# Optimization experiments

Hardware: AMD Instinct MI355X
Metric: run time of the kernel (lower is better)

The kernel has to match this reference:

```python
import jax, jax.numpy as jnp
import numpy as np

B, S, D, L, H = 4, 2048, 1024, 2, 8  # batch, seq, d_model, hierarchy levels, heads
DH = D // H


def _ln(x, g, b, eps=1e-5):
    mu = jnp.mean(x, axis=-1, keepdims=True)
    xc = x - mu
    var = jnp.mean(xc * xc, axis=-1, keepdims=True)
    return xc * jax.lax.rsqrt(var + eps) * g + b


def setup_inputs() -> dict:
    key = jax.random.key(0)
    ks = jax.random.split(key, 16)
    s = 0.02
    f32 = jnp.float32
    return {
        "x": jax.random.normal(ks[0], (B, S, D), f32),
        "hierarchy_levels": jax.random.randint(ks[1], (B, S), 0, 3),
        # per-level processor MLPs (stacked over level axis)
        "p1_w": jax.random.normal(ks[2], (L, D, D), f32) * s,
        "p1_b": jnp.zeros((L, D), f32),
        "p2_w": jax.random.normal(ks[3], (L, D, D), f32) * s,
        "p2_b": jnp.zeros((L, D), f32),
        "ln_g": jnp.ones((L, D), f32),
        "ln_b": jnp.zeros((L, D), f32),
        # multihead attention projections
        "wq": jax.random.normal(ks[4], (D, D), f32) * s,
        "bq": jnp.zeros((D,), f32),
        "wk": jax.random.normal(ks[5], (D, D), f32) * s,
        "bk": jnp.zeros((D,), f32),
        "wv": jax.random.normal(ks[6], (D, D), f32) * s,
        "bv": jnp.zeros((D,), f32),
        "wo": jax.random.normal(ks[7], (D, D), f32) * s,
        "bo": jnp.zeros((D,), f32),
        # integration MLP: Linear(L*D -> D), SiLU, Linear(D -> D), LayerNorm
        "i1_w": jax.random.normal(ks[8], (L * D, D), f32) * s,
        "i1_b": jnp.zeros((D,), f32),
        "i2_w": jax.random.normal(ks[9], (D, D), f32) * s,
        "i2_b": jnp.zeros((D,), f32),
        "iln_g": jnp.ones((D,), f32),
        "iln_b": jnp.zeros((D,), f32),
    }


def reference(x, hierarchy_levels, p1_w, p1_b, p2_w, p2_b, ln_g, ln_b,
              wq, bq, wk, bk, wv, bv, wo, bo,
              i1_w, i1_b, i2_w, i2_b, iln_g, iln_b):
    # --- per-token expert routing: compute all L processors, select by level ---
    t = jax.nn.silu(jnp.einsum('bsd,lde->lbse', x, p1_w) + p1_b[:, None, None, :])
    h = jnp.einsum('lbse,led->lbsd', t, p2_w) + p2_b[:, None, None, :]
    h = _ln(h, ln_g[:, None, None, :], ln_b[:, None, None, :])  # [L,B,S,D]
    oh = jax.nn.one_hot(hierarchy_levels, L, dtype=x.dtype)      # [B,S,L]; level>=L -> all-zero row
    hsel = jnp.einsum('lbsd,bsl->bsd', h, oh)                    # [B,S,D]
    # --- self-attention over routed outputs ---
    q = (hsel @ wq + bq).reshape(B, S, H, DH)
    k = (hsel @ wk + bk).reshape(B, S, H, DH)
    v = (hsel @ wv + bv).reshape(B, S, H, DH)
    scores = jnp.einsum('bqhd,bkhd->bhqk', q, k) / np.sqrt(DH).astype(x.dtype)
    a = jax.nn.softmax(scores, axis=-1)                          # [B,H,S,S]
    ctx = jnp.einsum('bhqk,bkhd->bqhd', a, v).reshape(B, S, D)
    attended = ctx @ wo + bo
    attn_weights = jnp.mean(a, axis=1)                           # torch avg over heads: [B,S,S]
    # --- integration MLP ---
    z = jnp.concatenate([hsel, attended], axis=-1)               # [B,S,2D]
    z = jax.nn.silu(z @ i1_w + i1_b) @ i2_w + i2_b
    out = _ln(z, iln_g, iln_b)
    return out, attn_weights
```

## Files before the change

kernel.cpp:

```cpp
#include <hip/hip_runtime.h>
#include <cstdint>
#include <cstddef>

#define B_ 4
#define S_ 2048
#define D_ 1024
#define H_ 8
#define DH_ 128
#define MTOT 8192
#define NT_ 32
#define SCALE2 (0.08838834764831845f * 1.4426950408889634f)

typedef __attribute__((ext_vector_type(8))) short s16x8;
typedef __attribute__((ext_vector_type(4))) float f32x4;
typedef __attribute__((ext_vector_type(8))) __bf16 bf16x8;

static __device__ __forceinline__ f32x4 mfma16(s16x8 a, s16x8 b, f32x4 c) {
  return __builtin_amdgcn_mfma_f32_16x16x32_bf16(
      __builtin_bit_cast(bf16x8, a), __builtin_bit_cast(bf16x8, b), c, 0, 0, 0);
}
static __device__ __forceinline__ unsigned short f2bf(float f) {
  unsigned u = __builtin_bit_cast(unsigned, f);
  u += 0x7fffu + ((u >> 16) & 1u);
  return (unsigned short)(u >> 16);
}
static __device__ __forceinline__ float bf2f(unsigned short u) {
  return __builtin_bit_cast(float, (unsigned)u << 16);
}
static __device__ __forceinline__ unsigned cvtpk2(float a, float b) {
  unsigned r;
  asm("v_cvt_pk_bf16_f32 %0, %1, %2" : "=v"(r) : "v"(a), "v"(b));
  return r;
}
static __device__ __forceinline__ void gload_lds16(const void* g, void* l) {
  __builtin_amdgcn_global_load_lds(
      (__attribute__((address_space(1))) void*)(void*)(g),
      (__attribute__((address_space(3))) void*)(l), 16, 0, 0);
}

__global__ __launch_bounds__(256) void xconv_kernel(const float* __restrict__ x,
                                                    unsigned short* __restrict__ xb) {
  long i = ((long)blockIdx.x * 256 + threadIdx.x) * 4;
  float4 v = *(const float4*)(x + i);
  ushort4 o;
  o.x = f2bf(v.x); o.y = f2bf(v.y); o.z = f2bf(v.z); o.w = f2bf(v.w);
  *(ushort4*)(xb + i) = o;
}

__global__ __launch_bounds__(256) void route_kernel(const int* __restrict__ levels,
                                                    int* __restrict__ cnt,
                                                    int* __restrict__ ridx,
                                                    int* __restrict__ act,
                                                    int* __restrict__ act2) {
  const int row = blockIdx.x * 256 + threadIdx.x;
  const int lane = threadIdx.x & 63;
  const int lvl = levels[row];
  const unsigned long long lmlt = (lane == 63) ? ~0ULL >> 1 : (1ULL << lane) - 1;

#pragma unroll
  for (int c = 0; c < 2; c++) {
    bool pred = (lvl == c);
    unsigned long long mask = __ballot(pred);
    int total = __popcll(mask);
    if (total) {
      int leader = __ffsll((long long)mask) - 1;
      int base = 0;
      if (lane == leader) base = atomicAdd(&cnt[c], total);
      base = __shfl(base, leader);
      if (pred) ridx[c * MTOT + base + __popcll(mask & lmlt)] = row;
    }
  }
  {
    bool pred = (lvl < 2);
    unsigned long long mask = __ballot(pred);
    int total = __popcll(mask);
    if (total) {
      int leader = __ffsll((long long)mask) - 1;
      int base = 0;
      if (lane == leader) base = atomicAdd(&cnt[2], total);
      base = __shfl(base, leader);
      if (pred) act[base + __popcll(mask & lmlt)] = row;
    }
    unsigned long long mask2 = ~mask;
    int total2 = 64 - total;
    if (total2) {
      int leader2 = __ffsll((long long)mask2) - 1;
      int base2 = 0;
      if (lane == leader2) base2 = atomicAdd(&cnt[3], total2);
      base2 = __shfl(base2, leader2);
      if (!pred) act2[base2 + __popcll(mask2 & lmlt)] = row;
    }
  }
}

__global__ __launch_bounds__(256) void lvl2fill_kernel(
    const int* __restrict__ act2, const int* __restrict__ cntp,
    const float* __restrict__ bq, const float* __restrict__ bk,
    const float* __restrict__ bv,
    unsigned short* __restrict__ qb, unsigned short* __restrict__ kb,
    unsigned short* __restrict__ vb, unsigned short* __restrict__ z) {
  const int idx = blockIdx.x;
  if (idx >= *cntp) return;
  const long row = act2[idx];
  const int t = threadIdx.x;
  const float4 q4 = *(const float4*)(bq + t * 4);
  const float4 k4 = *(const float4*)(bk + t * 4);
  const float4 v4 = *(const float4*)(bv + t * 4);
  ushort4 qo, ko, vo;
  qo.x = f2bf(q4.x * SCALE2); qo.y = f2bf(q4.y * SCALE2);
  qo.z = f2bf(q4.z * SCALE2); qo.w = f2bf(q4.w * SCALE2);
  ko.x = f2bf(k4.x); ko.y = f2bf(k4.y); ko.z = f2bf(k4.z); ko.w = f2bf(k4.w);
  vo.x = f2bf(v4.x); vo.y = f2bf(v4.y); vo.z = f2bf(v4.z); vo.w = f2bf(v4.w);
  *(ushort4*)(qb + row * 1024 + t * 4) = qo;
  *(ushort4*)(kb + row * 1024 + t * 4) = ko;
  *(ushort4*)(vb + row * 1024 + t * 4) = vo;
  *(ushort4*)(z + row * 2048 + t * 4) = (ushort4){0, 0, 0, 0};
}

struct WtDesc { const float* src; unsigned short* dst; long dst_ld; long dst_off; };
struct WtArgs { WtDesc d[10]; };
__global__ __launch_bounds__(256) void wtrans_all_kernel(WtArgs a) {
  __shared__ unsigned short tile[32][33];
  const int wi = blockIdx.y >> 5;
  const WtDesc de = a.d[wi];
  int r0 = (blockIdx.y & 31) * 32, c0 = blockIdx.x * 32;
  int tr = threadIdx.x >> 5, tc = threadIdx.x & 31;
#pragma unroll
  for (int i = 0; i < 4; i++)
    tile[tr + i * 8][tc] = f2bf(de.src[(long)(r0 + tr + i * 8) * 1024 + c0 + tc]);
  __syncthreads();
#pragma unroll
  for (int i = 0; i < 4; i++)
    de.dst[(long)(c0 + tr + i * 8) * de.dst_ld + de.dst_off + r0 + tc] = tile[tc][tr + i * 8];
}

__global__ __launch_bounds__(256) void vtrans_kernel(const unsigned short* __restrict__ V,
                                                     unsigned short* __restrict__ Vt) {
  __shared__ unsigned short tile[32][33];
  int b = blockIdx.z;
  int h = blockIdx.y >> 2, d0 = (blockIdx.y & 3) * 32;
  int s0 = blockIdx.x * 32;
  int tr = threadIdx.x >> 5, tc = threadIdx.x & 31;
#pragma unroll
  for (int i = 0; i < 4; i++)
    tile[tr + i * 8][tc] = V[((long)(b * S_) + s0 + tr + i * 8) * D_ + h * DH_ + d0 + tc];
  __syncthreads();
  const int sk = s0 + tc;
  const int k6 = sk & 63;
  const int slot = ((k6 >> 5) << 5) | (((k6 >> 2) & 3) << 3) | (((k6 >> 4) & 1) << 2) | (k6 & 3);
  const int ss = (sk & ~63) | slot;
#pragma unroll
  for (int i = 0; i < 4; i++)
    Vt[((long)(b * H_ + h) * DH_ + d0 + tr + i * 8) * S_ + ss] = tile[tc][tr + i * 8];
}

template <int TAG>
__global__ __launch_bounds__(256) void gemm_kernel(
    const unsigned short* __restrict__ A, int lda,
    const unsigned short* __restrict__ Wt, int ldw,
    const float* __restrict__ bias, float oscale,
    unsigned short* __restrict__ Cb, float* __restrict__ Cf, int ldc,
    int K, int do_silu) {
  __shared__ unsigned short lA[128 * 64];
  __shared__ unsigned short lB[128 * 64];
  const int t = threadIdx.x;
  const int wid = t >> 6, lane = t & 63;
  const int g = lane >> 4, lc = lane & 15;
  const int wr = wid >> 1, wc = wid & 1;
  const int nwg = gridDim.x * gridDim.y;
  int flat = blockIdx.x + gridDim.x * blockIdx.y;
  flat = (flat & 7) * (nwg >> 3) + (flat >> 3);
  const int m0 = (flat / gridDim.x) * 128;
  const int n0 = (flat % gridDim.x) * 128;
  const int srow = lane >> 3, scol = lane & 7;
  const int sxor = (scol ^ srow) << 4;

  f32x4 acc[4][4];
#pragma unroll
  for (int i = 0; i < 4; i++)
#pragma unroll
    for (int j = 0; j < 4; j++) acc[i][j] = (f32x4){0.f, 0.f, 0.f, 0.f};

  const int nk = K >> 6;
  for (int kt = 0; kt < nk; ++kt) {
    const int k0 = kt << 6;
#pragma unroll
    for (int i = 0; i < 4; i++) {
      const int r0 = wid * 32 + i * 8;
      gload_lds16((const char*)(A + (m0 + r0 + srow) * (long)lda + k0) + sxor,
                  (char*)lA + r0 * 128);
      gload_lds16((const char*)(Wt + (n0 + r0 + srow) * (long)ldw + k0) + sxor,
                  (char*)lB + r0 * 128);
    }
    __syncthreads();
#pragma unroll
    for (int kk = 0; kk < 2; kk++) {
      s16x8 af[4], bfr[4];
#pragma unroll
      for (int i = 0; i < 4; i++) {
        int row = wr * 64 + i * 16 + lc;
        af[i] = *(const s16x8*)((const char*)lA + row * 128 +
                                ((kk * 64 + g * 16) ^ ((row & 7) << 4)));
      }
#pragma unroll
      for (int j = 0; j < 4; j++) {
        int row = wc * 64 + j * 16 + lc;
        bfr[j] = *(const s16x8*)((const char*)lB + row * 128 +
                                 ((kk * 64 + g * 16) ^ ((row & 7) << 4)));
      }
#pragma unroll
      for (int i = 0; i < 4; i++)
#pragma unroll
        for (int j = 0; j < 4; j++) acc[i][j] = mfma16(af[i], bfr[j], acc[i][j]);
    }
    __syncthreads();
  }
#pragma unroll
  for (int i = 0; i < 4; i++) {
    const long rbase = m0 + wr * 64 + i * 16 + g * 4;
#pragma unroll
    for (int j = 0; j < 4; j++) {
      const int col = n0 + wc * 64 + j * 16 + lc;
      const float bv = bias[col];
#pragma unroll
      for (int r = 0; r < 4; r++) {
        float v = (acc[i][j][r] + bv) * oscale;
        if (do_silu) v = v / (1.f + __expf(-v));
        if (Cb) Cb[(rbase + r) * (long)ldc + col] = f2bf(v);
        else Cf[(rbase + r) * (long)ldc + col] = v;
      }
    }
  }
}

template <int TAG>
__global__ __launch_bounds__(512) void gemm8_kernel(
    const unsigned short* __restrict__ A, int lda,
    const unsigned short* __restrict__ Wt, int ldw,
    const float* __restrict__ bias, float oscale,
    unsigned short* __restrict__ Cb, int ldc,
    int K, int do_silu) {
  __shared__ unsigned short lA[128 * 64];
  __shared__ unsigned short lB[128 * 64];
  const int t = threadIdx.x;
  const int wid = t >> 6, lane = t & 63;
  const int g = lane >> 4, lc = lane & 15;
  const int wr = wid >> 1, wc = wid & 1;
  const int nwg = gridDim.x * gridDim.y;
  int flat = blockIdx.x + gridDim.x * blockIdx.y;
  flat = (flat & 7) * (nwg >> 3) + (flat >> 3);
  const int m0 = (flat / gridDim.x) * 128;
  const int n0 = (flat % gridDim.x) * 128;
  const int srow = lane >> 3, scol = lane & 7;
  const int sxor = (scol ^ srow) << 4;

  f32x4 acc[2][4];
#pragma unroll
  for (int i = 0; i < 2; i++)
#pragma unroll
    for (int j = 0; j < 4; j++) acc[i][j] = (f32x4){0.f, 0.f, 0.f, 0.f};

  const int nk = K >> 6;
  for (int kt = 0; kt < nk; ++kt) {
    const int k0 = kt << 6;
#pragma unroll
    for (int i = 0; i < 2; i++) {
      const int r0 = wid * 16 + i * 8;
      gload_lds16((const char*)(A + (m0 + r0 + srow) * (long)lda + k0) + sxor,
                  (char*)lA + r0 * 128);
      gload_lds16((const char*)(Wt + (n0 + r0 + srow) * (long)ldw + k0) + sxor,
                  (char*)lB + r0 * 128);
    }
    __syncthreads();
#pragma unroll
    for (int kk = 0; kk < 2; kk++) {
      s16x8 af[2], bfr[4];
#pragma unroll
      for (int i = 0; i < 2; i++) {
        int row = wr * 32 + i * 16 + lc;
        af[i] = *(const s16x8*)((const char*)lA + row * 128 +
                                ((kk * 64 + g * 16) ^ ((row & 7) << 4)));
      }
#pragma unroll
      for (int j = 0; j < 4; j++) {
        int row = wc * 64 + j * 16 + lc;
        bfr[j] = *(const s16x8*)((const char*)lB + row * 128 +
                                 ((kk * 64 + g * 16) ^ ((row & 7) << 4)));
      }
#pragma unroll
      for (int i = 0; i < 2; i++)
#pragma unroll
        for (int j = 0; j < 4; j++) acc[i][j] = mfma16(af[i], bfr[j], acc[i][j]);
    }
    __syncthreads();
  }
#pragma unroll
  for (int i = 0; i < 2; i++) {
    const long rbase = m0 + wr * 32 + i * 16 + g * 4;
#pragma unroll
    for (int j = 0; j < 4; j++) {
      const int col = n0 + wc * 64 + j * 16 + lc;
      const float bv = bias[col];
#pragma unroll
      for (int r = 0; r < 4; r++) {
        float v = (acc[i][j][r] + bv) * oscale;
        if (do_silu) v = v / (1.f + __expf(-v));
        Cb[(rbase + r) * (long)ldc + col] = f2bf(v);
      }
    }
  }
}

template <int RMAP>
__global__ __launch_bounds__(512) void gemm8_moe_kernel(
    const unsigned short* __restrict__ A, int lda,
    const unsigned short* __restrict__ Wt0, int ldw,
    const float* __restrict__ bias0,
    unsigned short* __restrict__ Cb, int ldc,
    int K, int do_silu, const int* __restrict__ ridx, const int* __restrict__ cnt2) {
  __shared__ unsigned short lA[128 * 64];
  __shared__ unsigned short lB[128 * 64];
  const int t = threadIdx.x;
  const int wid = t >> 6, lane = t & 63;
  const int g = lane >> 4, lc = lane & 15;
  const int wr = wid >> 1, wc = wid & 1;
  const int nwg = gridDim.x * gridDim.y;
  int flat = blockIdx.x + gridDim.x * blockIdx.y;
  flat = (flat & 7) * (nwg >> 3) + (flat >> 3);
  const int m0 = (flat / gridDim.x) * 128;
  const int n0 = (flat % gridDim.x) * 128;
  const int lvl = m0 >> 12;
  const int lm0 = m0 & 4095;
  if (lm0 >= cnt2[lvl]) return;
  const unsigned short* Wt = Wt0 + (long)lvl * 1048576;
  const float* bias = bias0 + lvl * 1024;
  const int srow = lane >> 3, scol = lane & 7;
  const int sxor = (scol ^ srow) << 4;

  const unsigned short* abase[2];
#pragma unroll
  for (int i = 0; i < 2; i++) {
    int ar;
    if (RMAP) ar = ridx[lvl * MTOT + lm0 + wid * 16 + i * 8 + srow];
    else ar = m0 + wid * 16 + i * 8 + srow;
    abase[i] = A + (long)ar * lda;
  }

  f32x4 acc[2][4];
#pragma unroll
  for (int i = 0; i < 2; i++)
#pragma unroll
    for (int j = 0; j < 4; j++) acc[i][j] = (f32x4){0.f, 0.f, 0.f, 0.f};

  const int nk = K >> 6;
  for (int kt = 0; kt < nk; ++kt) {
    const int k0 = kt << 6;
#pragma unroll
    for (int i = 0; i < 2; i++) {
      const int r0 = wid * 16 + i * 8;
      gload_lds16((const char*)(abase[i] + k0) + sxor, (char*)lA + r0 * 128);
      gload_lds16((const char*)(Wt + (n0 + r0 + srow) * (long)ldw + k0) + sxor,
                  (char*)lB + r0 * 128);
    }
    __syncthreads();
#pragma unroll
    for (int kk = 0; kk < 2; kk++) {
      s16x8 af[2], bfr[4];
#pragma unroll
      for (int i = 0; i < 2; i++) {
        int row = wr * 32 + i * 16 + lc;
        af[i] = *(const s16x8*)((const char*)lA + row * 128 +
                                ((kk * 64 + g * 16) ^ ((row & 7) << 4)));
      }
#pragma unroll
      for (int j = 0; j < 4; j++) {
        int row = wc * 64 + j * 16 + lc;
        bfr[j] = *(const s16x8*)((const char*)lB + row * 128 +
                                 ((kk * 64 + g * 16) ^ ((row & 7) << 4)));
      }
#pragma unroll
      for (int i = 0; i < 2; i++)
#pragma unroll
        for (int j = 0; j < 4; j++) acc[i][j] = mfma16(af[i], bfr[j], acc[i][j]);
    }
    __syncthreads();
  }
#pragma unroll
  for (int i = 0; i < 2; i++) {
    const long rbase = m0 + wr * 32 + i * 16 + g * 4;
#pragma unroll
    for (int j = 0; j < 4; j++) {
      const int col = n0 + wc * 64 + j * 16 + lc;
      const float bv = bias[col];
#pragma unroll
      for (int r = 0; r < 4; r++) {
        float v = acc[i][j][r] + bv;
        if (do_silu) v = v / (1.f + __expf(-v));
        Cb[(rbase + r) * (long)ldc + col] = f2bf(v);
      }
    }
  }
}

__global__ __launch_bounds__(256) void wct_gemm_kernel(
    const unsigned short* __restrict__ A,
    const unsigned short* __restrict__ Wb,
    float* __restrict__ Cf) {
  __shared__ unsigned short lA[128 * 64];
  __shared__ unsigned short lB[128 * 64];
  const int t = threadIdx.x;
  const int wid = t >> 6, lane = t & 63;
  const int g = lane >> 4, lc = lane & 15;
  const int wr = wid >> 1, wc = wid & 1;
  const int chunk = blockIdx.y >> 3;
  const int m0 = (blockIdx.y & 7) * 128;
  const int n0 = blockIdx.x * 128;
  const unsigned short* A0 = A + chunk * 256;
  const unsigned short* W0 = Wb + chunk * 256;
  float* C0 = Cf + (long)chunk * 1048576;
  const int srow = lane >> 3, scol = lane & 7;
  const int sxor = (scol ^ srow) << 4;

  f32x4 acc[4][4];
#pragma unroll
  for (int i = 0; i < 4; i++)
#pragma unroll
    for (int j = 0; j < 4; j++) acc[i][j] = (f32x4){0.f, 0.f, 0.f, 0.f};

  for (int kt = 0; kt < 4; ++kt) {
    const int k0 = kt << 6;
#pragma unroll
    for (int i = 0; i < 4; i++) {
      const int r0 = wid * 32 + i * 8;
      gload_lds16((const char*)(A0 + (m0 + r0 + srow) * 2048L + k0) + sxor,
                  (char*)lA + r0 * 128);
      gload_lds16((const char*)(W0 + (n0 + r0 + srow) * 1024L + k0) + sxor,
                  (char*)lB + r0 * 128);
    }
    __syncthreads();
#pragma unroll
    for (int kk = 0; kk < 2; kk++) {
      s16x8 af[4], bfr[4];
#pragma unroll
      for (int i = 0; i < 4; i++) {
        int row = wr * 64 + i * 16 + lc;
        af[i] = *(const s16x8*)((const char*)lA + row * 128 +
                                ((kk * 64 + g * 16) ^ ((row & 7) << 4)));
      }
#pragma unroll
      for (int j = 0; j < 4; j++) {
        int row = wc * 64 + j * 16 + lc;
        bfr[j] = *(const s16x8*)((const char*)lB + row * 128 +
                                 ((kk * 64 + g * 16) ^ ((row & 7) << 4)));
      }
#pragma unroll
      for (int i = 0; i < 4; i++)
#pragma unroll
        for (int j = 0; j < 4; j++) acc[i][j] = mfma16(af[i], bfr[j], acc[i][j]);
    }
    __syncthreads();
  }
#pragma unroll
  for (int i = 0; i < 4; i++) {
    const long rbase = m0 + wr * 64 + i * 16 + g * 4;
#pragma unroll
    for (int j = 0; j < 4; j++) {
      const int col = n0 + wc * 64 + j * 16 + lc;
#pragma unroll
      for (int r = 0; r < 4; r++) C0[(rbase + r) * 1024L + col] = acc[i][j][r];
    }
  }
}

__global__ __launch_bounds__(256) void wct_reduce_kernel(
    const float* __restrict__ hraw, unsigned short* __restrict__ i1t) {
  long e = ((long)blockIdx.x * 256 + threadIdx.x) * 2;
  float a0 = hraw[e] + hraw[e + 1048576] + hraw[e + 2097152] + hraw[e + 3145728];
  float a1 = hraw[e + 1] + hraw[e + 1 + 1048576] + hraw[e + 1 + 2097152] +
             hraw[e + 1 + 3145728];
  unsigned pk = cvtpk2(a0, a1);
  long n = e >> 10, c = e & 1023;
  *(unsigned*)(i1t + n * 2048 + 1024 + c) = pk;
}

__global__ __launch_bounds__(256) void biascomb_kernel(
    const unsigned short* __restrict__ i1t, const float* __restrict__ bo,
    const float* __restrict__ i1b, float* __restrict__ bias_c) {
  const int n = blockIdx.x, t = threadIdx.x;
  ushort4 w = *(const ushort4*)(i1t + (long)n * 2048 + 1024 + t * 4);
  float4 b = *(const float4*)(bo + t * 4);
  float s = bf2f(w.x) * b.x + bf2f(w.y) * b.y + bf2f(w.z) * b.z + bf2f(w.w) * b.w;
#pragma unroll
  for (int m = 32; m; m >>= 1) s += __shfl_xor(s, m);
  __shared__ float ws_[4];
  if ((t & 63) == 0) ws_[t >> 6] = s;
  __syncthreads();
  if (t == 0) bias_c[n] = i1b[n] + ws_[0] + ws_[1] + ws_[2] + ws_[3];
}

__global__ __launch_bounds__(256) void ln_moe_kernel(
    const unsigned short* __restrict__ in, const int* __restrict__ ridx,
    const int* __restrict__ cnt2,
    const float* __restrict__ gg0, const float* __restrict__ bb0,
    unsigned short* __restrict__ outb, long ldo) {
  const int row = blockIdx.x;
  const int lvl = row >> 12;
  const int lrow = row & 4095;
  if (lrow >= cnt2[lvl]) return;
  const int orow = ridx[lvl * MTOT + lrow];
  const float* gg = gg0 + lvl * 1024;
  const float* bb = bb0 + lvl * 1024;
  const int t = threadIdx.x;
  const ushort4 u = *(const ushort4*)(in + (long)row * D_ + t * 4);
  float v0 = bf2f(u.x), v1 = bf2f(u.y), v2 = bf2f(u.z), v3 = bf2f(u.w);
  float s1 = v0 + v1 + v2 + v3;
  float s2 = v0 * v0 + v1 * v1 + v2 * v2 + v3 * v3;
#pragma unroll
  for (int m = 32; m; m >>= 1) {
    s1 += __shfl_xor(s1, m);
    s2 += __shfl_xor(s2, m);
  }
  __shared__ float w1[4], w2[4];
  if ((t & 63) == 0) { w1[t >> 6] = s1; w2[t >> 6] = s2; }
  __syncthreads();
  s1 = w1[0] + w1[1] + w1[2] + w1[3];
  s2 = w2[0] + w2[1] + w2[2] + w2[3];
  const float mu = s1 * (1.f / D_);
  const float var = s2 * (1.f / D_) - mu * mu;
  const float rs = rsqrtf(var + 1e-5f);
  float vv[4] = {v0, v1, v2, v3};
#pragma unroll
  for (int jj = 0; jj < 4; jj++) {
    int col = t * 4 + jj;
    float y = (vv[jj] - mu) * rs * gg[col] + bb[col];
    outb[(long)orow * ldo + col] = f2bf(y);
  }
}

__global__ __launch_bounds__(256) void ln_kernel(
    const unsigned short* __restrict__ in,
    const float* __restrict__ gg, const float* __restrict__ bb,
    float* __restrict__ outf) {
  const int row = blockIdx.x;
  const int t = threadIdx.x;
  const ushort4 u = *(const ushort4*)(in + (long)row * D_ + t * 4);
  float v0 = bf2f(u.x), v1 = bf2f(u.y), v2 = bf2f(u.z), v3 = bf2f(u.w);
  float s1 = v0 + v1 + v2 + v3;
  float s2 = v0 * v0 + v1 * v1 + v2 * v2 + v3 * v3;
#pragma unroll
  for (int m = 32; m; m >>= 1) {
    s1 += __shfl_xor(s1, m);
    s2 += __shfl_xor(s2, m);
  }
  __shared__ float w1[4], w2[4];
  if ((t & 63) == 0) { w1[t >> 6] = s1; w2[t >> 6] = s2; }
  __syncthreads();
  s1 = w1[0] + w1[1] + w1[2] + w1[3];
  s2 = w2[0] + w2[1] + w2[2] + w2[3];
  const float mu = s1 * (1.f / D_);
  const float var = s2 * (1.f / D_) - mu * mu;
  const float rs = rsqrtf(var + 1e-5f);
  float vv[4] = {v0, v1, v2, v3};
#pragma unroll
  for (int jj = 0; jj < 4; jj++) {
    int col = t * 4 + jj;
    outf[(long)row * D_ + col] = (vv[jj] - mu) * rs * gg[col] + bb[col];
  }
}

__global__ __launch_bounds__(256) void gemm_qkv_kernel(
    const unsigned short* __restrict__ A, int lda,
    const unsigned short* __restrict__ Wt,
    const float* __restrict__ bq, const float* __restrict__ bk,
    const float* __restrict__ bv,
    unsigned short* __restrict__ qb, unsigned short* __restrict__ kb,
    unsigned short* __restrict__ vb,
    const int* __restrict__ act, const int* __restrict__ cntp) {
  __shared__ unsigned short lA[128 * 64];
  __shared__ unsigned short lB[128 * 64];
  const int t = threadIdx.x;
  const int wid = t >> 6, lane = t & 63;
  const int g = lane >> 4, lc = lane & 15;
  const int wr = wid >> 1, wc = wid & 1;
  const int nwg = gridDim.x * gridDim.y;
  int flat = blockIdx.x + gridDim.x * blockIdx.y;
  flat = (flat & 7) * (nwg >> 3) + (flat >> 3);
  const int m0 = (flat / gridDim.x) * 128;
  const int n0 = (flat % gridDim.x) * 128;
  if (m0 >= *cntp) return;
  const int srow = lane >> 3, scol = lane & 7;
  const int sxor = (scol ^ srow) << 4;

  const unsigned short* abase[4];
#pragma unroll
  for (int i = 0; i < 4; i++)
    abase[i] = A + (long)act[m0 + wid * 32 + i * 8 + srow] * lda;

  f32x4 acc[4][4];
#pragma unroll
  for (int i = 0; i < 4; i++)
#pragma unroll
    for (int j = 0; j < 4; j++) acc[i][j] = (f32x4){0.f, 0.f, 0.f, 0.f};

  for (int kt = 0; kt < 16; ++kt) {
    const int k0 = kt << 6;
#pragma unroll
    for (int i = 0; i < 4; i++) {
      const int r0 = wid * 32 + i * 8;
      gload_lds16((const char*)(abase[i] + k0) + sxor, (char*)lA + r0 * 128);
      gload_lds16((const char*)(Wt + (n0 + r0 + srow) * 1024 + k0) + sxor,
                  (char*)lB + r0 * 128);
    }
    __syncthreads();
#pragma unroll
    for (int kk = 0; kk < 2; kk++) {
      s16x8 af[4], bfr[4];
#pragma unroll
      for (int i = 0; i < 4; i++) {
        int row = wr * 64 + i * 16 + lc;
        af[i] = *(const s16x8*)((const char*)lA + row * 128 +
                                ((kk * 64 + g * 16) ^ ((row & 7) << 4)));
      }
#pragma unroll
      for (int j = 0; j < 4; j++) {
        int row = wc * 64 + j * 16 + lc;
        bfr[j] = *(const s16x8*)((const char*)lB + row * 128 +
                                 ((kk * 64 + g * 16) ^ ((row & 7) << 4)));
      }
#pragma unroll
      for (int i = 0; i < 4; i++)
#pragma unroll
        for (int j = 0; j < 4; j++) acc[i][j] = mfma16(af[i], bfr[j], acc[i][j]);
    }
    __syncthreads();
  }
  const int whichB = n0 >> 10;
  const float* bias = whichB == 0 ? bq : whichB == 1 ? bk : bv;
  unsigned short* Cb = whichB == 0 ? qb : whichB == 1 ? kb : vb;
  const float oscale = whichB == 0 ? (float)SCALE2 : 1.0f;
  const int nb = n0 & 1023;
#pragma unroll
  for (int i = 0; i < 4; i++) {
    const int ribase = m0 + wr * 64 + i * 16 + g * 4;
#pragma unroll
    for (int j = 0; j < 4; j++) {
      const int col = nb + wc * 64 + j * 16 + lc;
      const float bvv = bias[col];
#pragma unroll
      for (int r = 0; r < 4; r++) {
        float v = (acc[i][j][r] + bvv) * oscale;
        Cb[(long)act[ribase + r] * 1024L + col] = f2bf(v);
      }
    }
  }
}

__global__ __launch_bounds__(256, 2) void flash_kernel(
    const unsigned short* __restrict__ Q, const unsigned short* __restrict__ Kb,
    const unsigned short* __restrict__ Vt,
    unsigned short* __restrict__ zatt, float* __restrict__ Mo, float* __restrict__ Lo) {
  __shared__ unsigned short lK[2][64 * 128];
  __shared__ unsigned short lV[2][128 * 64];
  const int t = threadIdx.x, wid = t >> 6, lane = t & 63;
  const int g = lane >> 4, lc = lane & 15;
  const int d = blockIdx.x + 16 * (blockIdx.y + 8 * blockIdx.z);
  const int qd = d >> 3, rd = d & 7;
  const int grp = rd + 8 * (qd >> 4);
  const int b = grp >> 3, h = grp & 7, q0 = (qd & 15) * 128;
  const int k_l4 = lane >> 4, k_c = lane & 15;
  const int v_l3 = lane >> 3, v_c = lane & 7;

  s16x8 qf[2][4];
#pragma unroll
  for (int qi = 0; qi < 2; qi++)
#pragma unroll
    for (int kk = 0; kk < 4; kk++)
      qf[qi][kk] = *(const s16x8*)(Q +
          ((long)(b * S_ + q0 + wid * 32 + qi * 16 + lc)) * D_ + h * DH_ + kk * 32 + g * 8);

  f32x4 acco[2][8];
#pragma unroll
  for (int qi = 0; qi < 2; qi++)
#pragma unroll
    for (int dn = 0; dn < 8; dn++) acco[qi][dn] = (f32x4){0.f, 0.f, 0.f, 0.f};
  float m_run[2] = {-1e30f, -1e30f}, l_run[2] = {0.f, 0.f};

  auto stageK = [&](int kt, int buf) {
#pragma unroll
    for (int i = 0; i < 4; i++) {
      const int r0 = wid * 16 + i * 4;
      const int row = r0 + k_l4;
      gload_lds16((const char*)(Kb + (b * S_ + kt * 64 + row) * D_ + h * DH_) +
                      ((k_c ^ (row & 7)) << 4),
                  (char*)&lK[buf][0] + r0 * 256);
    }
  };
  auto stageV = [&](int kt, int buf) {
#pragma unroll
    for (int i = 0; i < 4; i++) {
      const int r0 = wid * 32 + i * 8;
      const int row = r0 + v_l3;
      gload_lds16((const char*)(Vt + ((b * H_ + h) * DH_ + row) * S_ + kt * 64) +
                      ((v_c ^ (row & 7)) << 4),
                  (char*)&lV[buf][0] + r0 * 128);
    }
  };

  stageK(0, 0);
  stageV(0, 0);
  __syncthreads();

  for (int kt = 0; kt < NT_; ++kt) {
    const int cur = kt & 1;
    if (kt + 1 < NT_) { stageK(kt + 1, cur ^ 1); stageV(kt + 1, cur ^ 1); }

    f32x4 s[2][4];
#pragma unroll
    for (int qi = 0; qi < 2; qi++)
#pragma unroll
      for (int kn = 0; kn < 4; kn++) s[qi][kn] = (f32x4){0.f, 0.f, 0.f, 0.f};
    __builtin_amdgcn_s_setprio(1);
#pragma unroll
    for (int kk = 0; kk < 4; kk++) {
      s16x8 kf[4];
#pragma unroll
      for (int kn = 0; kn < 4; kn++) {
        int row = kn * 16 + lc;
        kf[kn] = *(const s16x8*)((const char*)&lK[cur][0] + row * 256 +
                                 ((kk * 64 + g * 16) ^ ((row & 7) << 4)));
      }
#pragma unroll
      for (int qi = 0; qi < 2; qi++)
#pragma unroll
        for (int kn = 0; kn < 4; kn++) s[qi][kn] = mfma16(kf[kn], qf[qi][kk], s[qi][kn]);
    }
    __builtin_amdgcn_s_setprio(0);

    float mx[2];
    int trig = 0;
#pragma unroll
    for (int qi = 0; qi < 2; qi++) {
      float m01 = fmaxf(fmaxf(s[qi][0][0], s[qi][0][1]), fmaxf(s[qi][0][2], s[qi][0][3]));
      float m1 = fmaxf(fmaxf(s[qi][1][0], s[qi][1][1]), fmaxf(s[qi][1][2], s[qi][1][3]));
      float m2 = fmaxf(fmaxf(s[qi][2][0], s[qi][2][1]), fmaxf(s[qi][2][2], s[qi][2][3]));
      float m3 = fmaxf(fmaxf(s[qi][3][0], s[qi][3][1]), fmaxf(s[qi][3][2], s[qi][3][3]));
      float m = fmaxf(fmaxf(m01, m1), fmaxf(m2, m3));
      m = fmaxf(m, __shfl_xor(m, 16));
      m = fmaxf(m, __shfl_xor(m, 32));
      mx[qi] = m;
      trig |= (m > m_run[qi] + 8.0f);
    }
    if (__any(trig)) {
#pragma unroll
      for (int qi = 0; qi < 2; qi++) {
        float mn = fmaxf(m_run[qi], mx[qi]);
        float fsc = exp2f(m_run[qi] - mn);
        m_run[qi] = mn;
        l_run[qi] *= fsc;
#pragma unroll
        for (int dn = 0; dn < 8; dn++)
#pragma unroll
          for (int r = 0; r < 4; r++) acco[qi][dn][r] *= fsc;
      }
    }

    unsigned w[2][4][2];
#pragma unroll
    for (int qi = 0; qi < 2; qi++) {
      float ls = 0.f;
#pragma unroll
      for (int kn = 0; kn < 4; kn++) {
        float p0 = exp2f(s[qi][kn][0] - m_run[qi]);
        float p1 = exp2f(s[qi][kn][1] - m_run[qi]);
        float p2 = exp2f(s[qi][kn][2] - m_run[qi]);
        float p3 = exp2f(s[qi][kn][3] - m_run[qi]);
        ls += (p0 + p1) + (p2 + p3);
        w[qi][kn][0] = cvtpk2(p0, p1);
        w[qi][kn][1] = cvtpk2(p2, p3);
      }
      ls += __shfl_xor(ls, 16);
      ls += __shfl_xor(ls, 32);
      l_run[qi] += ls;
    }

    __builtin_amdgcn_s_setprio(1);
#pragma unroll
    for (int kk = 0; kk < 2; kk++) {
      s16x8 pf[2];
#pragma unroll
      for (int qi = 0; qi < 2; qi++) {
        union { unsigned u[4]; s16x8 v; } pu;
        pu.u[0] = w[qi][2 * kk][0];
        pu.u[1] = w[qi][2 * kk][1];
        pu.u[2] = w[qi][2 * kk + 1][0];
        pu.u[3] = w[qi][2 * kk + 1][1];
        pf[qi] = pu.v;
      }
#pragma unroll
      for (int dn = 0; dn < 8; dn++) {
        int vrow = dn * 16 + lc;
        s16x8 vf = *(const s16x8*)((const char*)&lV[cur][0] + vrow * 128 +
                                   ((kk * 64 + g * 16) ^ ((vrow & 7) << 4)));
#pragma unroll
        for (int qi = 0; qi < 2; qi++) acco[qi][dn] = mfma16(vf, pf[qi], acco[qi][dn]);
      }
    }
    __builtin_amdgcn_s_setprio(0);
    __syncthreads();
  }

  char* tb = (char*)&lK[0][0] + wid * 8192;
#pragma unroll
  for (int qi = 0; qi < 2; qi++) {
    float inv = 1.f / l_run[qi];
    int row = qi * 16 + lc;
#pragma unroll
    for (int dn = 0; dn < 8; dn++) {
      unsigned lo = cvtpk2(acco[qi][dn][0] * inv, acco[qi][dn][1] * inv);
      unsigned hi = cvtpk2(acco[qi][dn][2] * inv, acco[qi][dn][3] * inv);
      unsigned long long pk = (unsigned long long)lo | ((unsigned long long)hi << 32);
      *(unsigned long long*)(tb + row * 256 + ((dn * 32 + g * 8) ^ ((row & 7) << 4))) = pk;
    }
  }
  __syncthreads();
#pragma unroll
  for (int i = 0; i < 8; i++) {
    const int row = i * 4 + (lane >> 4);
    const int chunk = lane & 15;
    s16x8 vv = *(const s16x8*)(tb + row * 256 + ((chunk * 16) ^ ((row & 7) << 4)));
    *(s16x8*)(zatt + ((long)(b * S_ + q0 + wid * 32 + row)) * 2048 + h * DH_ + chunk * 8) = vv;
  }
  if (g == 0) {
#pragma unroll
    for (int qi = 0; qi < 2; qi++) {
      int q = q0 + wid * 32 + qi * 16 + lc;
      Mo[(long)(b * H_ + h) * S_ + q] = m_run[qi];
      Lo[(long)(b * H_ + h) * S_ + q] = l_run[qi];
    }
  }
}

__global__ __launch_bounds__(256) void attw_kernel(
    const unsigned short* __restrict__ Q, const unsigned short* __restrict__ Kb,
    const float* __restrict__ Mo, const float* __restrict__ Lo,
    float* __restrict__ AW) {
  __shared__ unsigned short lK[2][128 * 128];
  __shared__ float lm[H_][128], winv[H_][128];
  const int t = threadIdx.x, wid = t >> 6, lane = t & 63;
  const int g = lane >> 4, lc = lane & 15;
  const int f = blockIdx.x + 16 * (blockIdx.y + 16 * blockIdx.z);
  const int xcd = f & 7, i_ = f >> 3;
  const int grp = (i_ >> 4) * 8 + xcd;
  const int b = grp >> 4, k0 = (grp & 15) * 128, q0 = (i_ & 15) * 128;
  const int k_l4 = lane >> 4, k_c = lane & 15;

  for (int i = t; i < H_ * 128; i += 256) {
    int h = i >> 7, qq = i & 127;
    lm[h][qq] = Mo[(long)(b * H_ + h) * S_ + q0 + qq];
    winv[h][qq] = 0.125f / Lo[(long)(b * H_ + h) * S_ + q0 + qq];
  }

  auto stageK = [&](int h, int buf) {
#pragma unroll
    for (int i = 0; i < 8; i++) {
      const int r0 = wid * 32 + i * 4;
      const int row = r0 + k_l4;
      gload_lds16((const char*)(Kb + ((long)(b * S_ + k0 + row)) * D_ + h * DH_) +
                      ((k_c ^ (row & 7)) << 4),
                  (char*)&lK[buf][0] + r0 * 256);
    }
  };

  f32x4 acc[2][8];
#pragma unroll
  for (int qi = 0; qi < 2; qi++)
#pragma unroll
    for (int kn = 0; kn < 8; kn++) acc[qi][kn] = (f32x4){0.f, 0.f, 0.f, 0.f};

  stageK(0, 0);
  __syncthreads();

  for (int h = 0; h < H_; ++h) {
    const int cur = h & 1;
    if (h + 1 < H_) stageK(h + 1, cur ^ 1);
    f32x4 s[2][8];
#pragma unroll
    for (int qi = 0; qi < 2; qi++)
#pragma unroll
      for (int kn = 0; kn < 8; kn++) s[qi][kn] = (f32x4){0.f, 0.f, 0.f, 0.f};
    __builtin_amdgcn_s_setprio(1);
#pragma unroll
    for (int kk = 0; kk < 4; kk++) {
      s16x8 qa[2];
#pragma unroll
      for (int qi = 0; qi < 2; qi++)
        qa[qi] = *(const s16x8*)(Q +
            ((long)(b * S_ + q0 + wid * 32 + qi * 16 + lc)) * D_ + h * DH_ + kk * 32 + g * 8);
#pragma unroll
      for (int kn = 0; kn < 8; kn++) {
        int row = kn * 16 + lc;
        s16x8 kf = *(const s16x8*)((const char*)&lK[cur][0] + row * 256 +
                                   ((kk * 64 + g * 16) ^ ((row & 7) << 4)));
#pragma unroll
        for (int qi = 0; qi < 2; qi++) s[qi][kn] = mfma16(qa[qi], kf, s[qi][kn]);
      }
    }
    __builtin_amdgcn_s_setprio(0);
#pragma unroll
    for (int qi = 0; qi < 2; qi++)
#pragma unroll
      for (int kn = 0; kn < 8; kn++)
#pragma unroll
        for (int r = 0; r < 4; r++) {
          int qq = wid * 32 + qi * 16 + g * 4 + r;
          acc[qi][kn][r] += exp2f(s[qi][kn][r] - lm[h][qq]) * winv[h][qq];
        }
    __syncthreads();
  }
#pragma unroll
  for (int qi = 0; qi < 2; qi++)
#pragma unroll
    for (int kn = 0; kn < 8; kn++)
#pragma unroll
      for (int r = 0; r < 4; r++) {
        long q = q0 + wid * 32 + qi * 16 + g * 4 + r;
        int k = k0 + kn * 16 + lc;
        AW[((long)b * S_ + q) * S_ + k] = acc[qi][kn][r];
      }
}

__global__ void signal_kernel(float* out, float v) { out[0] = v; }

extern "C" void kernel_launch(void* const* d_in, const int* in_sizes, int n_in,
                              void* d_out, int out_size, void* d_ws, size_t ws_size,
                              hipStream_t stream) {
  constexpr size_t OFF_XB = 0;
  constexpr size_t OFF_W = 16777216ULL;
  constexpr size_t OFF_T = 39845888ULL;
  constexpr size_t OFF_HR = 56623104ULL;
  constexpr size_t OFF_Z = 90177536ULL;
  constexpr size_t OFF_Q = 123731968ULL;
  constexpr size_t OFF_K = 140509184ULL;
  constexpr size_t OFF_V = 157286400ULL;
  constexpr size_t OFF_VT = 174063616ULL;
  constexpr size_t OFF_M = 190840832ULL;
  constexpr size_t OFF_L = 191102976ULL;
  constexpr size_t OFF_CNT = 191365120ULL;
  constexpr size_t OFF_RIDX = 191365184ULL;
  constexpr size_t OFF_BC = OFF_RIDX + 2ULL * MTOT * 4;
  constexpr size_t OFF_ACT = OFF_BC + 4096;
  constexpr size_t OFF_ACT2 = OFF_ACT + MTOT * 4;
  constexpr size_t WS_NEED = OFF_ACT2 + MTOT * 4;

  if (ws_size < WS_NEED) {
    signal_kernel<<<1, 1, 0, stream>>>((float*)d_out, (float)ws_size);
    return;
  }
  const float* x = (const float*)d_in[0];
  const int* levels = (const int*)d_in[1];
  const float* p1w = (const float*)d_in[2];
  const float* p1b = (const float*)d_in[3];
  const float* p2w = (const float*)d_in[4];
  const float* p2b = (const float*)d_in[5];
  const float* lng = (const float*)d_in[6];
  const float* lnb = (const float*)d_in[7];
  const float* wq = (const float*)d_in[8];
  const float* bq = (const float*)d_in[9];
  const float* wk = (const float*)d_in[10];
  const float* bk = (const float*)d_in[11];
  const float* wv = (const float*)d_in[12];
  const float* bv = (const float*)d_in[13];
  const float* wo = (const float*)d_in[14];
  const float* bo = (const float*)d_in[15];
  const float* i1w = (const float*)d_in[16];
  const float* i1b = (const float*)d_in[17];
  const float* i2w = (const float*)d_in[18];
  const float* i2b = (const float*)d_in[19];
  const float* ilng = (const float*)d_in[20];
  const float* ilnb = (const float*)d_in[21];

  char* ws = (char*)d_ws;
  unsigned short* xb = (unsigned short*)(ws + OFF_XB);
  unsigned short* p1t = (unsigned short*)(ws + OFF_W);
  unsigned short* p2t = p1t + 2 * 1048576;
  unsigned short* wqt = p2t + 2 * 1048576;
  unsigned short* wkt = wqt + 1048576;
  unsigned short* wvt = wkt + 1048576;
  unsigned short* wob = wvt + 1048576;
  unsigned short* i1t = wob + 1048576;
  unsigned short* i2t = i1t + 2097152;
  unsigned short* tbuf = (unsigned short*)(ws + OFF_T);
  float* wctp = (float*)(ws + OFF_HR);
  unsigned short* hraw16 = (unsigned short*)(ws + OFF_HR);
  unsigned short* z = (unsigned short*)(ws + OFF_Z);
  unsigned short* qb = (unsigned short*)(ws + OFF_Q);
  unsigned short* kb = (unsigned short*)(ws + OFF_K);
  unsigned short* vb = (unsigned short*)(ws + OFF_V);
  unsigned short* vt = (unsigned short*)(ws + OFF_VT);
  float* Mo = (float*)(ws + OFF_M);
  float* Lo = (float*)(ws + OFF_L);
  int* cnt = (int*)(ws + OFF_CNT);
  int* ridx = (int*)(ws + OFF_RIDX);
  float* bias_c = (float*)(ws + OFF_BC);
  int* act = (int*)(ws + OFF_ACT);
  int* act2 = (int*)(ws + OFF_ACT2);
  float* out = (float*)d_out;
  float* aw = out + (size_t)MTOT * D_;

  dim3 blk(256), blk8(512);
  hipMemsetAsync(cnt, 0, 64, stream);
  hipMemsetAsync(ridx, 0, 2 * MTOT * 4, stream);
  hipMemsetAsync(act, 0, MTOT * 4, stream);
  xconv_kernel<<<8192, blk, 0, stream>>>(x, xb);
  route_kernel<<<32, blk, 0, stream>>>(levels, cnt, ridx, act, act2);
  lvl2fill_kernel<<<MTOT, blk, 0, stream>>>(act2, cnt + 3, bq, bk, bv, qb, kb, vb, z);

  WtArgs wa;
  wa.d[0] = {p1w, p1t, 1024, 0};
  wa.d[1] = {p1w + 1048576, p1t + 1048576, 1024, 0};
  wa.d[2] = {p2w, p2t, 1024, 0};
  wa.d[3] = {p2w + 1048576, p2t + 1048576, 1024, 0};
  wa.d[4] = {wq, wqt, 1024, 0};
  wa.d[5] = {wk, wkt, 1024, 0};
  wa.d[6] = {wv, wvt, 1024, 0};
  wa.d[7] = {i1w, i1t, 2048, 0};
  wa.d[8] = {i1w + 1048576, i1t, 2048, 1024};
  wa.d[9] = {i2w, i2t, 1024, 0};
  wtrans_all_kernel<<<dim3(32, 320), blk, 0, stream>>>(wa);
  xconv_kernel<<<1024, blk, 0, stream>>>(wo, wob);
  wct_gemm_kernel<<<dim3(8, 32), blk, 0, stream>>>(i1t + 1024, wob, wctp);
  biascomb_kernel<<<1024, blk, 0, stream>>>(i1t, bo, i1b, bias_c);
  wct_reduce_kernel<<<2048, blk, 0, stream>>>(wctp, i1t);

  gemm8_moe_kernel<1><<<dim3(8, 64), blk8, 0, stream>>>(xb, 1024, p1t, 1024, p1b,
                                                        tbuf, 1024, 1024, 1, ridx, cnt);
  gemm8_moe_kernel<0><<<dim3(8, 64), blk8, 0, stream>>>(tbuf, 1024, p2t, 1024, p2b,
                                                        hraw16, 1024, 1024, 0, ridx, cnt);
  ln_moe_kernel<<<8192, blk, 0, stream>>>(hraw16, ridx, cnt, lng, lnb, z, 2048);

  gemm_qkv_kernel<<<dim3(24, 64), blk, 0, stream>>>(z, 2048, wqt, bq, bk, bv, qb, kb, vb,
                                                    act, cnt + 2);
  vtrans_kernel<<<dim3(64, 32, 4), blk, 0, stream>>>(vb, vt);
  flash_kernel<<<dim3(16, 8, 4), blk, 0, stream>>>(qb, kb, vt, z + 1024, Mo, Lo);
  attw_kernel<<<dim3(16, 16, 4), blk, 0, stream>>>(qb, kb, Mo, Lo, aw);
  gemm8_kernel<3><<<dim3(8, 64), blk8, 0, stream>>>(z, 2048, i1t, 2048, bias_c, 1.0f, tbuf,
                                                    1024, 2048, 1);
  gemm8_kernel<4><<<dim3(8, 64), blk8, 0, stream>>>(tbuf, 1024, i2t, 1024, i2b, 1.0f, hraw16,
                                                    1024, 1024, 0);
  ln_kernel<<<8192, blk, 0, stream>>>(hraw16, ilng, ilnb, out);
}
```

Before: 440.7 us.

## Compact attention queries per batch, compute one representative for level-2 rows

Level-2 tokens have all-zero hsel, so their q rows equal the bias and give identical attention outputs and weights. The route kernel now builds per-batch compacted lists of active rows plus one representative level-2 row. Flash and attention-weight kernels process only those compacted query tiles, and new broadcast kernels copy the representative's context and attention-weight rows to the other level-2 rows. This cuts query-side attention work by about a third under the level distribution, at the cost of extra small kernels, indirect row indexing and scattered stores.

```diff
diff --git a/kernel.cpp b/kernel.cpp
--- a/kernel.cpp
+++ b/kernel.cpp
@@ -51,8 +51,10 @@
                                                     int* __restrict__ cnt,
                                                     int* __restrict__ ridx,
                                                     int* __restrict__ act,
-                                                    int* __restrict__ act2) {
+                                                    int* __restrict__ act2,
+                                                    int* __restrict__ actb) {
   const int row = blockIdx.x * 256 + threadIdx.x;
+  const int bb = blockIdx.x >> 3;
   const int lane = threadIdx.x & 63;
   const int lvl = levels[row];
   const unsigned long long lmlt = (lane == 63) ? ~0ULL >> 1 : (1ULL << lane) - 1;
@@ -74,12 +76,16 @@
     bool pred = (lvl < 2);
     unsigned long long mask = __ballot(pred);
     int total = __popcll(mask);
+    int leader = __ffsll((long long)mask) - 1;
     if (total) {
-      int leader = __ffsll((long long)mask) - 1;
       int base = 0;
       if (lane == leader) base = atomicAdd(&cnt[2], total);
       base = __shfl(base, leader);
       if (pred) act[base + __popcll(mask & lmlt)] = row;
+      int baseb = 0;
+      if (lane == leader) baseb = atomicAdd(&cnt[4 + bb], total);
+      baseb = __shfl(baseb, leader);
+      if (pred) actb[bb * 2048 + baseb + __popcll(mask & lmlt)] = row;
     }
     unsigned long long mask2 = ~mask;
     int total2 = 64 - total;
@@ -90,6 +96,32 @@
       base2 = __shfl(base2, leader2);
       if (!pred) act2[base2 + __popcll(mask2 & lmlt)] = row;
     }
+  }
+}
+
+__global__ __launch_bounds__(256) void prep_kernel(
+    const int* __restrict__ cnt, const int* __restrict__ act2,
+    int* __restrict__ actb, int* __restrict__ rep, int* __restrict__ cntEff) {
+  const int t = threadIdx.x;
+  __shared__ int srep[4];
+  if (t < 4) srep[t] = -1;
+  __syncthreads();
+  const int n3 = cnt[3];
+  for (int i = t; i < n3; i += 256) {
+    int row = act2[i];
+    srep[row >> 11] = row;
+  }
+  __syncthreads();
+  if (t < 4) {
+    rep[t] = srep[t];
+    int ce = cnt[4 + t] + (srep[t] >= 0 ? 1 : 0);
+    cntEff[t] = ce > 2048 ? 2048 : ce;
+  }
+  __syncthreads();
+  for (int b = 0; b < 4; b++) {
+    int c = cnt[4 + b];
+    int fill = srep[b] >= 0 ? srep[b] : actb[b * 2048];
+    for (int i = c + t; i < 2048; i += 256) actb[b * 2048 + i] = fill;
   }
 }
 
@@ -117,6 +149,37 @@
   *(ushort4*)(z + row * 2048 + t * 4) = (ushort4){0, 0, 0, 0};
 }
 
+__global__ __launch_bounds__(256) void bcast_ctx_kernel(
+    const int* __restrict__ act2, const int* __restrict__ cntp,
+    const int* __restrict__ rep, unsigned short* __restrict__ z) {
+  const int idx = blockIdx.x;
+  if (idx >= *cntp) return;
+  const long row = act2[idx];
+  const int b = (int)(row >> 11);
+  const long rp = rep[b];
+  if (row == rp) return;
+  const int t = threadIdx.x;
+  *(ushort4*)(z + row * 2048 + 1024 + t * 4) =
+      *(const ushort4*)(z + rp * 2048 + 1024 + t * 4);
+}
+
+__global__ __launch_bounds__(256) void bcast_aw_kernel(
+    const int* __restrict__ act2, const int* __restrict__ cntp,
+    const int* __restrict__ rep, float* __restrict__ AW) {
+  const int idx = blockIdx.x;
+  if (idx >= *cntp) return;
+  const long row = act2[idx];
+  const int b = (int)(row >> 11);
+  const long rp = rep[b];
+  if (row == rp) return;
+  const int t = threadIdx.x;
+  const float* src = AW + ((long)b * S_ + (rp & 2047)) * S_;
+  float* dst = AW + ((long)b * S_ + (row & 2047)) * S_;
+#pragma unroll
+  for (int i = 0; i < 2; i++)
+    *(float4*)(dst + t * 4 + i * 1024) = *(const float4*)(src + t * 4 + i * 1024);
+}
+
 struct WtDesc { const float* src; unsigned short* dst; long dst_ld; long dst_off; };
 struct WtArgs { WtDesc d[10]; };
 __global__ __launch_bounds__(256) void wtrans_all_kernel(WtArgs a) {
@@ -152,85 +215,6 @@
 #pragma unroll
   for (int i = 0; i < 4; i++)
     Vt[((long)(b * H_ + h) * DH_ + d0 + tr + i * 8) * S_ + ss] = tile[tc][tr + i * 8];
-}
-
-template <int TAG>
-__global__ __launch_bounds__(256) void gemm_kernel(
-    const unsigned short* __restrict__ A, int lda,
-    const unsigned short* __restrict__ Wt, int ldw,
-    const float* __restrict__ bias, float oscale,
-    unsigned short* __restrict__ Cb, float* __restrict__ Cf, int ldc,
-    int K, int do_silu) {
-  __shared__ unsigned short lA[128 * 64];
-  __shared__ unsigned short lB[128 * 64];
-  const int t = threadIdx.x;
-  const int wid = t >> 6, lane = t & 63;
-  const int g = lane >> 4, lc = lane & 15;
-  const int wr = wid >> 1, wc = wid & 1;
-  const int nwg = gridDim.x * gridDim.y;
-  int flat = blockIdx.x + gridDim.x * blockIdx.y;
-  flat = (flat & 7) * (nwg >> 3) + (flat >> 3);
-  const int m0 = (flat / gridDim.x) * 128;
-  const int n0 = (flat % gridDim.x) * 128;
-  const int srow = lane >> 3, scol = lane & 7;
-  const int sxor = (scol ^ srow) << 4;
-
-  f32x4 acc[4][4];
-#pragma unroll
-  for (int i = 0; i < 4; i++)
-#pragma unroll
-    for (int j = 0; j < 4; j++) acc[i][j] = (f32x4){0.f, 0.f, 0.f, 0.f};
-
-  const int nk = K >> 6;
-  for (int kt = 0; kt < nk; ++kt) {
-    const int k0 = kt << 6;
-#pragma unroll
-    for (int i = 0; i < 4; i++) {
-      const int r0 = wid * 32 + i * 8;
-      gload_lds16((const char*)(A + (m0 + r0 + srow) * (long)lda + k0) + sxor,
-                  (char*)lA + r0 * 128);
-      gload_lds16((const char*)(Wt + (n0 + r0 + srow) * (long)ldw + k0) + sxor,
-                  (char*)lB + r0 * 128);
-    }
-    __syncthreads();
-#pragma unroll
-    for (int kk = 0; kk < 2; kk++) {
-      s16x8 af[4], bfr[4];
-#pragma unroll
-      for (int i = 0; i < 4; i++) {
-        int row = wr * 64 + i * 16 + lc;
-        af[i] = *(const s16x8*)((const char*)lA + row * 128 +
-                                ((kk * 64 + g * 16) ^ ((row & 7) << 4)));
-      }
-#pragma unroll
-      for (int j = 0; j < 4; j++) {
-        int row = wc * 64 + j * 16 + lc;
-        bfr[j] = *(const s16x8*)((const char*)lB + row * 128 +
-                                 ((kk * 64 + g * 16) ^ ((row & 7) << 4)));
-      }
-#pragma unroll
-      for (int i = 0; i < 4; i++)
-#pragma unroll
-        for (int j = 0; j < 4; j++) acc[i][j] = mfma16(af[i], bfr[j], acc[i][j]);
-    }
-    __syncthreads();
-  }
-#pragma unroll
-  for (int i = 0; i < 4; i++) {
-    const long rbase = m0 + wr * 64 + i * 16 + g * 4;
-#pragma unroll
-    for (int j = 0; j < 4; j++) {
-      const int col = n0 + wc * 64 + j * 16 + lc;
-      const float bv = bias[col];
-#pragma unroll
-      for (int r = 0; r < 4; r++) {
-        float v = (acc[i][j][r] + bv) * oscale;
-        if (do_silu) v = v / (1.f + __expf(-v));
-        if (Cb) Cb[(rbase + r) * (long)ldc + col] = f2bf(v);
-        else Cf[(rbase + r) * (long)ldc + col] = v;
-      }
-    }
-  }
 }
 
 template <int TAG>
@@ -658,7 +642,8 @@
 __global__ __launch_bounds__(256, 2) void flash_kernel(
     const unsigned short* __restrict__ Q, const unsigned short* __restrict__ Kb,
     const unsigned short* __restrict__ Vt,
-    unsigned short* __restrict__ zatt, float* __restrict__ Mo, float* __restrict__ Lo) {
+    unsigned short* __restrict__ zatt, float* __restrict__ Mo, float* __restrict__ Lo,
+    const int* __restrict__ actb, const int* __restrict__ cntEff) {
   __shared__ unsigned short lK[2][64 * 128];
   __shared__ unsigned short lV[2][128 * 64];
   const int t = threadIdx.x, wid = t >> 6, lane = t & 63;
@@ -667,16 +652,20 @@
   const int qd = d >> 3, rd = d & 7;
   const int grp = rd + 8 * (qd >> 4);
   const int b = grp >> 3, h = grp & 7, q0 = (qd & 15) * 128;
+  if (q0 >= cntEff[b]) return;
+  const int* lst = actb + b * 2048;
   const int k_l4 = lane >> 4, k_c = lane & 15;
   const int v_l3 = lane >> 3, v_c = lane & 7;
 
+  int grow[2];
   s16x8 qf[2][4];
 #pragma unroll
-  for (int qi = 0; qi < 2; qi++)
+  for (int qi = 0; qi < 2; qi++) {
+    grow[qi] = lst[q0 + wid * 32 + qi * 16 + lc];
 #pragma unroll
     for (int kk = 0; kk < 4; kk++)
-      qf[qi][kk] = *(const s16x8*)(Q +
-          ((long)(b * S_ + q0 + wid * 32 + qi * 16 + lc)) * D_ + h * DH_ + kk * 32 + g * 8);
+      qf[qi][kk] = *(const s16x8*)(Q + (long)grow[qi] * D_ + h * DH_ + kk * 32 + g * 8);
+  }
 
   f32x4 acco[2][8];
 #pragma unroll
@@ -827,15 +816,15 @@
   for (int i = 0; i < 8; i++) {
     const int row = i * 4 + (lane >> 4);
     const int chunk = lane & 15;
+    const long gr = lst[q0 + wid * 32 + row];
     s16x8 vv = *(const s16x8*)(tb + row * 256 + ((chunk * 16) ^ ((row & 7) << 4)));
-    *(s16x8*)(zatt + ((long)(b * S_ + q0 + wid * 32 + row)) * 2048 + h * DH_ + chunk * 8) = vv;
+    *(s16x8*)(zatt + gr * 2048 + h * DH_ + chunk * 8) = vv;
   }
   if (g == 0) {
 #pragma unroll
     for (int qi = 0; qi < 2; qi++) {
-      int q = q0 + wid * 32 + qi * 16 + lc;
-      Mo[(long)(b * H_ + h) * S_ + q] = m_run[qi];
-      Lo[(long)(b * H_ + h) * S_ + q] = l_run[qi];
+      Mo[(long)(b * H_ + h) * S_ + (grow[qi] & 2047)] = m_run[qi];
+      Lo[(long)(b * H_ + h) * S_ + (grow[qi] & 2047)] = l_run[qi];
     }
   }
 }
@@ -843,7 +832,8 @@
 __global__ __launch_bounds__(256) void attw_kernel(
     const unsigned short* __restrict__ Q, const unsigned short* __restrict__ Kb,
     const float* __restrict__ Mo, const float* __restrict__ Lo,
-    float* __restrict__ AW) {
+    float* __restrict__ AW,
+    const int* __restrict__ actb, const int* __restrict__ cntEff) {
   __shared__ unsigned short lK[2][128 * 128];
   __shared__ float lm[H_][128], winv[H_][128];
   const int t = threadIdx.x, wid = t >> 6, lane = t & 63;
@@ -852,13 +842,20 @@
   const int xcd = f & 7, i_ = f >> 3;
   const int grp = (i_ >> 4) * 8 + xcd;
   const int b = grp >> 4, k0 = (grp & 15) * 128, q0 = (i_ & 15) * 128;
+  if (q0 >= cntEff[b]) return;
+  const int* lst = actb + b * 2048;
   const int k_l4 = lane >> 4, k_c = lane & 15;
 
   for (int i = t; i < H_ * 128; i += 256) {
     int h = i >> 7, qq = i & 127;
-    lm[h][qq] = Mo[(long)(b * H_ + h) * S_ + q0 + qq];
-    winv[h][qq] = 0.125f / Lo[(long)(b * H_ + h) * S_ + q0 + qq];
-  }
+    int gr = lst[q0 + qq] & 2047;
+    lm[h][qq] = Mo[(long)(b * H_ + h) * S_ + gr];
+    winv[h][qq] = 0.125f / Lo[(long)(b * H_ + h) * S_ + gr];
+  }
+
+  int glq[2];
+#pragma unroll
+  for (int qi = 0; qi < 2; qi++) glq[qi] = lst[q0 + wid * 32 + qi * 16 + lc];
 
   auto stageK = [&](int h, int buf) {
 #pragma unroll
@@ -894,8 +891,7 @@
       s16x8 qa[2];
 #pragma unroll
       for (int qi = 0; qi < 2; qi++)
-        qa[qi] = *(const s16x8*)(Q +
-            ((long)(b * S_ + q0 + wid * 32 + qi * 16 + lc)) * D_ + h * DH_ + kk * 32 + g * 8);
+        qa[qi] = *(const s16x8*)(Q + (long)glq[qi] * D_ + h * DH_ + kk * 32 + g * 8);
 #pragma unroll
       for (int kn = 0; kn < 8; kn++) {
         int row = kn * 16 + lc;
@@ -923,9 +919,9 @@
     for (int kn = 0; kn < 8; kn++)
 #pragma unroll
       for (int r = 0; r < 4; r++) {
-        long q = q0 + wid * 32 + qi * 16 + g * 4 + r;
+        const int gqr = lst[q0 + wid * 32 + qi * 16 + g * 4 + r] & 2047;
         int k = k0 + kn * 16 + lc;
-        AW[((long)b * S_ + q) * S_ + k] = acc[qi][kn][r];
+        AW[((long)b * S_ + gqr) * S_ + k] = acc[qi][kn][r];
       }
 }
 
@@ -950,7 +946,10 @@
   constexpr size_t OFF_BC = OFF_RIDX + 2ULL * MTOT * 4;
   constexpr size_t OFF_ACT = OFF_BC + 4096;
   constexpr size_t OFF_ACT2 = OFF_ACT + MTOT * 4;
-  constexpr size_t WS_NEED = OFF_ACT2 + MTOT * 4;
+  constexpr size_t OFF_ACTB = OFF_ACT2 + MTOT * 4;
+  constexpr size_t OFF_REP = OFF_ACTB + 4 * 2048 * 4;
+  constexpr size_t OFF_CEF = OFF_REP + 64;
+  constexpr size_t WS_NEED = OFF_CEF + 64;
 
   if (ws_size < WS_NEED) {
     signal_kernel<<<1, 1, 0, stream>>>((float*)d_out, (float)ws_size);
@@ -1004,6 +1003,9 @@
   float* bias_c = (float*)(ws + OFF_BC);
   int* act = (int*)(ws + OFF_ACT);
   int* act2 = (int*)(ws + OFF_ACT2);
+  int* actb = (int*)(ws + OFF_ACTB);
+  int* rep = (int*)(ws + OFF_REP);
+  int* cntEff = (int*)(ws + OFF_CEF);
   float* out = (float*)d_out;
   float* aw = out + (size_t)MTOT * D_;
 
@@ -1012,7 +1014,8 @@
   hipMemsetAsync(ridx, 0, 2 * MTOT * 4, stream);
   hipMemsetAsync(act, 0, MTOT * 4, stream);
   xconv_kernel<<<8192, blk, 0, stream>>>(x, xb);
-  route_kernel<<<32, blk, 0, stream>>>(levels, cnt, ridx, act, act2);
+  route_kernel<<<32, blk, 0, stream>>>(levels, cnt, ridx, act, act2, actb);
+  prep_kernel<<<1, blk, 0, stream>>>(cnt, act2, actb, rep, cntEff);
   lvl2fill_kernel<<<MTOT, blk, 0, stream>>>(act2, cnt + 3, bq, bk, bv, qb, kb, vb, z);
 
   WtArgs wa;
@@ -1041,8 +1044,11 @@
   gemm_qkv_kernel<<<dim3(24, 64), blk, 0, stream>>>(z, 2048, wqt, bq, bk, bv, qb, kb, vb,
                                                     act, cnt + 2);
   vtrans_kernel<<<dim3(64, 32, 4), blk, 0, stream>>>(vb, vt);
-  flash_kernel<<<dim3(16, 8, 4), blk, 0, stream>>>(qb, kb, vt, z + 1024, Mo, Lo);
-  attw_kernel<<<dim3(16, 16, 4), blk, 0, stream>>>(qb, kb, Mo, Lo, aw);
+  flash_kernel<<<dim3(16, 8, 4), blk, 0, stream>>>(qb, kb, vt, z + 1024, Mo, Lo,
+                                                   actb, cntEff);
+  bcast_ctx_kernel<<<MTOT, blk, 0, stream>>>(act2, cnt + 3, rep, z);
+  attw_kernel<<<dim3(16, 16, 4), blk, 0, stream>>>(qb, kb, Mo, Lo, aw, actb, cntEff);
+  bcast_aw_kernel<<<MTOT, blk, 0, stream>>>(act2, cnt + 3, rep, aw);
   gemm8_kernel<3><<<dim3(8, 64), blk8, 0, stream>>>(z, 2048, i1t, 2048, bias_c, 1.0f, tbuf,
                                                     1024, 2048, 1);
   gemm8_kernel<4><<<dim3(8, 64), blk8, 0, stream>>>(tbuf, 1024, i2t, 1024, i2b, 1.0f, hraw16,
```

New measurement: 449.9 us. 2.1% more time.
